# Optimization experiments

Hardware: AMD Instinct MI355X
Metric: run time of the kernel (lower is better)

The kernel has to match this reference:

```python
import jax, jax.numpy as jnp
import numpy as np

C = 1.0          # ball curvature c (manifold k = -c)
RC = 1.0         # sqrt(c)
PROJ_EPS = 4e-3  # geoopt float32 projection eps
NUM_HEADS = 16
B, S, D = 2, 1024, 1024


def _project(x):
    # clip points back inside the Poincare ball
    maxnorm = (1.0 - PROJ_EPS) / RC
    norm = jnp.maximum(jnp.linalg.norm(x, axis=-1, keepdims=True), 1e-15)
    return jnp.where(norm > maxnorm, x / norm * maxnorm, x)


def _poincare_linear(x, z, r, out_split):
    # Unidirectional Poincare MLR (Shimizu et al., HNN++) followed by exp-map back to the ball.
    # x: [..., din]; z: [din, dout]; r: [dout]
    z_norm = jnp.maximum(jnp.linalg.norm(z, axis=0, keepdims=True), 1e-15)  # [1, dout]
    z_unit = z / z_norm
    drcr = 2.0 * RC * r                                    # [dout]
    rcx = RC * x
    cx2 = jnp.sum(rcx * rcx, axis=-1, keepdims=True)       # [..., 1]
    w = 2.0 * (z_norm / RC) * jnp.arcsinh(
        (2.0 * (rcx @ z_unit) * jnp.cosh(drcr) - (1.0 + cx2) * jnp.sinh(drcr))
        / jnp.maximum(1.0 - cx2, 1e-15))
    y = jnp.sinh(RC * w) / RC
    y = y.reshape(y.shape[:-1] + (out_split, y.shape[-1] // out_split))  # [..., H, dh]
    y = _project(y)
    y = y / (1.0 + jnp.sqrt(1.0 + C * jnp.sum(y * y, axis=-1, keepdims=True)))
    return _project(y)


def _dist_matmul(x, y):
    # Pairwise Poincare distance via matmul. x: [..., n, d], y: [..., d, m].
    # dist = (1/sqrt(c)) * arccosh(1 + 2c||x-y||^2 / ((1-c||x||^2)(1-c||y||^2)))
    xy = jnp.matmul(x, y)
    x2 = jnp.sum(x * x, axis=-1, keepdims=True)           # [..., n, 1]
    y2 = jnp.sum(y * y, axis=-2, keepdims=True)           # [..., 1, m]
    num = jnp.maximum(x2 - 2.0 * xy + y2, 1e-15)          # ||x - y||^2
    den = jnp.maximum((1.0 - C * x2) * (1.0 - C * y2), 1e-15)
    return (1.0 / RC) * jnp.arccosh(1.0 + 2.0 * C * num / den)


def _weighted_midpoint_bmm(xs, weights):
    # Weighted Mobius gyromidpoint. xs: [..., n, d], weights: [..., m, n] -> [..., m, d]
    x2 = jnp.sum(xs * xs, axis=-1, keepdims=True)
    gamma = 2.0 / jnp.maximum(1.0 - C * x2, 1e-15)        # conformal factor lambda_x
    denom = jnp.matmul(jnp.abs(weights), gamma - 1.0)     # [..., m, 1]
    nomin = jnp.matmul(weights, gamma * xs)               # [..., m, d]
    two_mean = nomin / jnp.maximum(denom, 1e-10)
    sq = jnp.sum(two_mean * two_mean, axis=-1, keepdims=True)
    a_mean = two_mean / (1.0 + jnp.sqrt(jnp.maximum(1.0 - C * sq, 1e-15)))
    return _project(a_mean)


def setup_inputs() -> dict:
    key = jax.random.key(0)
    ks = jax.random.split(key, 4)
    # points must lie inside the unit ball: ||x|| ~ 0.02*sqrt(D) ~ 0.64
    hidden_states = 0.02 * jax.random.normal(ks[0], (B, S, D), dtype=jnp.float32)
    attention_mask = jnp.zeros((B, 1, 1, S), dtype=jnp.float32)
    scale = 1.0 / np.sqrt(D).astype(np.float32)
    qz = scale * jax.random.normal(ks[1], (D, D), dtype=jnp.float32)
    kz = scale * jax.random.normal(ks[2], (D, D), dtype=jnp.float32)
    vz = scale * jax.random.normal(ks[3], (D, D), dtype=jnp.float32)
    qr = jnp.zeros((D,), jnp.float32)
    kr = jnp.zeros((D,), jnp.float32)
    vr = jnp.zeros((D,), jnp.float32)
    return {"hidden_states": hidden_states, "attention_mask": attention_mask,
            "qz": qz, "qr": qr, "kz": kz, "kr": kr, "vz": vz, "vr": vr}


def reference(hidden_states, attention_mask, qz, qr, kz, kr, vz, vr):
    # self-attention path (encoder_hidden_states is None), eval mode (dropout p=0)
    q = _poincare_linear(hidden_states, qz, qr, NUM_HEADS).transpose(0, 2, 1, 3)  # [B,H,S,dh]
    k = _poincare_linear(hidden_states, kz, kr, NUM_HEADS).transpose(0, 2, 1, 3)
    v = _poincare_linear(hidden_states, vz, vr, NUM_HEADS).transpose(0, 2, 1, 3)
    scores = -_dist_matmul(q, jnp.swapaxes(k, -1, -2)) + attention_mask          # [B,H,S,S]
    probs = jax.nn.softmax(scores, axis=-1)
    ctx = _weighted_midpoint_bmm(v, probs)                                       # [B,H,S,dh]
    b, h, s, dh = ctx.shape
    return ctx.transpose(0, 2, 1, 3).reshape(b, s, h * dh)
```

## Files before the change

kernel.cpp:

```cpp
#include <hip/hip_runtime.h>
#include <math.h>

#define BB 2
#define SS 1024
#define DD 1024
#define NH 16
#define DH 64
#define MAXN 0.996f

typedef __attribute__((ext_vector_type(8))) short bf16x8;
typedef __attribute__((ext_vector_type(4))) float f32x4;

__device__ __forceinline__ float xor_sum16(float v){
  v += __shfl_xor(v, 1, 64);
  v += __shfl_xor(v, 2, 64);
  v += __shfl_xor(v, 4, 64);
  v += __shfl_xor(v, 8, 64);
  return v;
}

__device__ __forceinline__ unsigned short f2bf(float x){
  unsigned u = __builtin_bit_cast(unsigned, x);
  unsigned r = u + 0x7FFFu + ((u >> 16) & 1u);
  return (unsigned short)(r >> 16);
}
__device__ __forceinline__ float bf2f(unsigned short b){
  unsigned u = ((unsigned)b) << 16;
  return __builtin_bit_cast(float, u);
}

__device__ __forceinline__ void async_copy16(const unsigned short* g, unsigned short* s){
  __builtin_amdgcn_global_load_lds(
      (const __attribute__((address_space(1))) unsigned int*)g,
      (__attribute__((address_space(3))) unsigned int*)s,
      16, 0, 0);
}

__global__ __launch_bounds__(256) void col_stats_kernel(
    const float* __restrict__ zq, const float* __restrict__ zk, const float* __restrict__ zv,
    const float* __restrict__ rq, const float* __restrict__ rk, const float* __restrict__ rv,
    float* __restrict__ acol, float* __restrict__ bcol, float* __restrict__ scol)
{
  const int m = blockIdx.y;
  const float* z = (m == 0) ? zq : ((m == 1) ? zk : zv);
  const float* r = (m == 0) ? rq : ((m == 1) ? rk : rv);
  const int col = blockIdx.x * 64 + (threadIdx.x & 63);
  const int slice = threadIdx.x >> 6;
  float acc = 0.0f;
  for (int i = slice * 256; i < slice * 256 + 256; ++i) {
    float t = z[(size_t)i * DD + col]; acc = fmaf(t, t, acc);
  }
  __shared__ float red[4][64];
  red[slice][threadIdx.x & 63] = acc;
  __syncthreads();
  if (slice == 0) {
    const int c = threadIdx.x & 63;
    float a = red[0][c] + red[1][c] + red[2][c] + red[3][c];
    float n = fmaxf(sqrtf(a), 1e-15f);
    float rr = 2.0f * r[col];
    acol[m * DD + col] = 2.0f * coshf(rr) / n;
    bcol[m * DD + col] = sinhf(rr);
    scol[m * DD + col] = 2.0f * n;
  }
}

__global__ __launch_bounds__(256) void row_cx2_kernel(const float* __restrict__ x,
                                                      float* __restrict__ cx2)
{
  const int wave = threadIdx.x >> 6;
  const int lane = threadIdx.x & 63;
  const int row = blockIdx.x * 4 + wave;
  const float* xr = x + (size_t)row * DD;
  float acc = 0.0f;
  for (int i = lane; i < DD; i += 64) { float t = xr[i]; acc = fmaf(t, t, acc); }
  #pragma unroll
  for (int m = 1; m < 64; m <<= 1) acc += __shfl_xor(acc, m, 64);
  if (lane == 0) cx2[row] = acc;
}

__global__ __launch_bounds__(256) void convert_x_kernel(
    const float* __restrict__ x,
    unsigned short* __restrict__ Xhi, unsigned short* __restrict__ Xlo)
{
  const size_t g0 = ((size_t)blockIdx.x * 256 + threadIdx.x) * 8;
  #pragma unroll
  for (int h = 0; h < 2; ++h) {
    float4 v = *(const float4*)(x + g0 + 4 * h);
    float a[4] = {v.x, v.y, v.z, v.w};
    ushort4 hv, lv;
    unsigned short* hp = (unsigned short*)&hv;
    unsigned short* lp = (unsigned short*)&lv;
    #pragma unroll
    for (int j = 0; j < 4; ++j) {
      unsigned short hi = f2bf(a[j]);
      hp[j] = hi;
      lp[j] = f2bf(a[j] - bf2f(hi));
    }
    *(ushort4*)(Xhi + g0 + 4 * h) = hv;
    *(ushort4*)(Xlo + g0 + 4 * h) = lv;
  }
}

__global__ __launch_bounds__(256) void convert_zt_kernel(
    const float* __restrict__ zq, const float* __restrict__ zk, const float* __restrict__ zv,
    unsigned short* __restrict__ ZThi, unsigned short* __restrict__ ZTlo)
{
  const int kt = blockIdx.x, nt = blockIdx.y, mat = blockIdx.z;
  const float* z = (mat == 0) ? zq : ((mat == 1) ? zk : zv);
  const int tid = threadIdx.x;
  __shared__ unsigned T[64][69];

  #pragma unroll
  for (int i = 0; i < 4; ++i) {
    const int g = tid + 256 * i;
    const int kr = g >> 4, nc = (g & 15) * 4;
    float4 v = *(const float4*)(z + (size_t)(kt * 64 + kr) * DD + nt * 64 + nc);
    float a[4] = {v.x, v.y, v.z, v.w};
    #pragma unroll
    for (int j = 0; j < 4; ++j) {
      unsigned short hi = f2bf(a[j]);
      unsigned short lo = f2bf(a[j] - bf2f(hi));
      T[kr][nc + j] = ((unsigned)lo << 16) | (unsigned)hi;
    }
  }
  __syncthreads();
  #pragma unroll
  for (int i = 0; i < 4; ++i) {
    const int g = tid + 256 * i;
    const int nr = g >> 4, kc = (g & 15) * 4;
    ushort4 hv, lv;
    unsigned short* hp = (unsigned short*)&hv;
    unsigned short* lp = (unsigned short*)&lv;
    #pragma unroll
    for (int j = 0; j < 4; ++j) {
      unsigned u = T[kc + j][nr];
      hp[j] = (unsigned short)(u & 0xFFFFu);
      lp[j] = (unsigned short)(u >> 16);
    }
    const size_t ob = ((size_t)mat * DD + nt * 64 + nr) * DD + kt * 64 + kc;
    *(ushort4*)(ZThi + ob) = hv;
    *(ushort4*)(ZTlo + ob) = lv;
  }
}

__global__ __launch_bounds__(256, 3) void gemm_mfma_kernel(
    const unsigned short* __restrict__ Xhi, const unsigned short* __restrict__ Xlo,
    const unsigned short* __restrict__ ZThi, const unsigned short* __restrict__ ZTlo,
    const float* __restrict__ acol, const float* __restrict__ bcol, const float* __restrict__ scol,
    const float* __restrict__ cx2,
    float* __restrict__ Q, float* __restrict__ K, float* __restrict__ GV,
    float* __restrict__ q2, float* __restrict__ k2, float* __restrict__ gm1)
{
  __shared__ unsigned short S[2][12288];

  const int mat = blockIdx.z;
  float* OutM = (mat == 0) ? Q  : ((mat == 1) ? K  : GV);
  float* Stat = (mat == 0) ? q2 : ((mat == 1) ? k2 : gm1);

  const int n0 = blockIdx.x * 128;
  const int m0 = blockIdx.y * 64;
  const int tid = threadIdx.x;
  const int wave = tid >> 6, lane = tid & 63;
  const int tx = lane & 15, quad = lane >> 4;
  const int wrow = wave & 1;
  const int wcol = wave >> 1;

  const int l4r = lane >> 2, l4c = (lane & 3) * 8;
  auto slice_ptr = [&](int si) -> const unsigned short* {
    if (si < 8) {
      const unsigned short* base = (si < 4) ? Xhi : Xlo;
      const int r16 = (si & 3) * 16;
      return base + (size_t)(m0 + r16 + l4r) * DD + l4c;
    } else {
      const unsigned short* base = (si < 16) ? ZThi : ZTlo;
      const int r16 = ((si - 8) & 7) * 16;
      return base + ((size_t)mat * DD + n0 + r16 + l4r) * DD + l4c;
    }
  };
  const int s0 = 6 * wave;
  const unsigned short* p0 = slice_ptr(s0 + 0);
  const unsigned short* p1 = slice_ptr(s0 + 1);
  const unsigned short* p2 = slice_ptr(s0 + 2);
  const unsigned short* p3 = slice_ptr(s0 + 3);
  const unsigned short* p4 = slice_ptr(s0 + 4);
  const unsigned short* p5 = slice_ptr(s0 + 5);
  const int o0 = 512 * (s0 + 0), o1 = 512 * (s0 + 1), o2 = 512 * (s0 + 2);
  const int o3 = 512 * (s0 + 3), o4 = 512 * (s0 + 4), o5 = 512 * (s0 + 5);

  const f32x4 z4 = {0.f, 0.f, 0.f, 0.f};
  f32x4 d00 = z4, d01 = z4, d02 = z4, d03 = z4;
  f32x4 d10 = z4, d11 = z4, d12 = z4, d13 = z4;

  async_copy16(p0, &S[0][o0]); async_copy16(p1, &S[0][o1]); async_copy16(p2, &S[0][o2]);
  async_copy16(p3, &S[0][o3]); async_copy16(p4, &S[0][o4]); async_copy16(p5, &S[0][o5]);
  p0 += 32; p1 += 32; p2 += 32; p3 += 32; p4 += 32; p5 += 32;

  for (int kt = 0; kt < 32; ++kt) {
    __syncthreads();
    if (kt < 31) {
      unsigned short* Bn = S[(kt + 1) & 1];
      async_copy16(p0, Bn + o0); async_copy16(p1, Bn + o1); async_copy16(p2, Bn + o2);
      async_copy16(p3, Bn + o3); async_copy16(p4, Bn + o4); async_copy16(p5, Bn + o5);
      p0 += 32; p1 += 32; p2 += 32; p3 += 32; p4 += 32; p5 += 32;
    }
    const unsigned short* Bc = S[kt & 1];
    const int ar = 32 * wrow + tx;
    bf16x8 a_h0 = *(const bf16x8*)&Bc[ar * 32 + 8 * quad];
    bf16x8 a_l0 = *(const bf16x8*)&Bc[2048 + ar * 32 + 8 * quad];
    bf16x8 a_h1 = *(const bf16x8*)&Bc[(ar + 16) * 32 + 8 * quad];
    bf16x8 a_l1 = *(const bf16x8*)&Bc[2048 + (ar + 16) * 32 + 8 * quad];

#define DO_NB(NB, C0, C1) { \
      const int brow = 16 * (4 * wcol + NB) + tx; \
      bf16x8 b_h = *(const bf16x8*)&Bc[4096 + brow * 32 + 8 * quad]; \
      bf16x8 b_l = *(const bf16x8*)&Bc[8192 + brow * 32 + 8 * quad]; \
      C0 = __builtin_amdgcn_mfma_f32_16x16x32_bf16(a_h0, b_h, C0, 0, 0, 0); \
      C0 = __builtin_amdgcn_mfma_f32_16x16x32_bf16(a_h0, b_l, C0, 0, 0, 0); \
      C0 = __builtin_amdgcn_mfma_f32_16x16x32_bf16(a_l0, b_h, C0, 0, 0, 0); \
      C1 = __builtin_amdgcn_mfma_f32_16x16x32_bf16(a_h1, b_h, C1, 0, 0, 0); \
      C1 = __builtin_amdgcn_mfma_f32_16x16x32_bf16(a_h1, b_l, C1, 0, 0, 0); \
      C1 = __builtin_amdgcn_mfma_f32_16x16x32_bf16(a_l1, b_h, C1, 0, 0, 0); }
    DO_NB(0, d00, d10)
    DO_NB(1, d01, d11)
    DO_NB(2, d02, d12)
    DO_NB(3, d03, d13)
#undef DO_NB
  }

  const int head = blockIdx.x * 2 + wcol;
  #pragma unroll
  for (int mb = 0; mb < 2; ++mb) {
    const f32x4 e0 = mb ? d10 : d00;
    const f32x4 e1 = mb ? d11 : d01;
    const f32x4 e2 = mb ? d12 : d02;
    const f32x4 e3 = mb ? d13 : d03;
    #pragma unroll
    for (int r = 0; r < 4; ++r) {
      const int row = m0 + 32 * wrow + 16 * mb + 4 * quad + r;
      const float c2 = cx2[row];
      const float inv = 1.0f / fmaxf(1.0f - c2, 1e-15f);
      const float onec = 1.0f + c2;
      float yv[4];
      #pragma unroll
      for (int nb = 0; nb < 4; ++nb) {
        const float accv = (nb == 0) ? e0[r] : (nb == 1) ? e1[r] : (nb == 2) ? e2[r] : e3[r];
        const int col = mat * DD + n0 + 64 * wcol + 16 * nb + tx;
        const float u = fmaf(accv, acol[col], -(onec * bcol[col])) * inv;
        const float a = fabsf(u);
        const float t = a + sqrtf(fmaf(a, a, 1.0f));
        const float p = __builtin_amdgcn_exp2f(scol[col] * __builtin_amdgcn_logf(t));
        float y = 0.5f * (p - __builtin_amdgcn_rcpf(p));
        yv[nb] = copysignf(y, u);
      }
      const int b = row >> 10, s = row & 1023;
      float n2 = 0.f;
      #pragma unroll
      for (int j = 0; j < 4; ++j) n2 = fmaf(yv[j], yv[j], n2);
      n2 = xor_sum16(n2);
      float n = fmaxf(sqrtf(n2), 1e-15f);
      float s1 = (n > MAXN) ? (MAXN / n) : 1.0f;
      n2 = n2 * s1 * s1;
      float f = 1.0f / (1.0f + sqrtf(1.0f + n2));
      float fs = s1 * f;
      n2 = n2 * f * f;
      float nb2 = fmaxf(sqrtf(n2), 1e-15f);
      float s2f = (nb2 > MAXN) ? (MAXN / nb2) : 1.0f;
      fs *= s2f;
      n2 = n2 * s2f * s2f;

      const size_t bh = (size_t)(b * NH + head);
      const size_t outbase = (bh * SS + s) * DH;
      if (mat == 2) {
        const float gamma = 2.0f / fmaxf(1.0f - n2, 1e-15f);
        #pragma unroll
        for (int j = 0; j < 4; ++j)
          OutM[outbase + 16 * j + tx] = yv[j] * fs * gamma;
        if (tx == 0) Stat[bh * SS + s] = gamma - 1.0f;
      } else {
        #pragma unroll
        for (int j = 0; j < 4; ++j)
          OutM[outbase + 16 * j + tx] = yv[j] * fs;
        if (tx == 0) Stat[bh * SS + s] = n2;
      }
    }
  }
}

__global__ __launch_bounds__(256) void convert_kernel(
    const float* __restrict__ QKV,
    unsigned short* __restrict__ Qhi, unsigned short* __restrict__ Qlo,
    unsigned short* __restrict__ Khi, unsigned short* __restrict__ Klo,
    unsigned short* __restrict__ GThi, unsigned short* __restrict__ GTlo)
{
  const int st = blockIdx.x, bh = blockIdx.y, mat = blockIdx.z;
  const int tid = threadIdx.x;
  const size_t nQKV = (size_t)BB * NH * SS * DH;
  const float* src = QKV + (size_t)mat * nQKV + ((size_t)bh * SS + st * 64) * DH;
  __shared__ unsigned T[64][69];

  if (mat < 2) {
    unsigned short* dh_ = ((mat == 0) ? Qhi : Khi) + ((size_t)bh * SS + st * 64) * DH;
    unsigned short* dl_ = ((mat == 0) ? Qlo : Klo) + ((size_t)bh * SS + st * 64) * DH;
    #pragma unroll
    for (int i = 0; i < 4; ++i) {
      const int g = tid + 256 * i;
      const int row = g >> 4, c4 = (g & 15) * 4;
      float4 v = *(const float4*)(src + row * DH + c4);
      float a[4] = {v.x, v.y, v.z, v.w};
      ushort4 hv, lv;
      unsigned short* hp = (unsigned short*)&hv;
      unsigned short* lp = (unsigned short*)&lv;
      #pragma unroll
      for (int j = 0; j < 4; ++j) {
        unsigned short hi = f2bf(a[j]);
        hp[j] = hi;
        lp[j] = f2bf(a[j] - bf2f(hi));
      }
      *(ushort4*)(dh_ + row * DH + c4) = hv;
      *(ushort4*)(dl_ + row * DH + c4) = lv;
    }
  } else {
    #pragma unroll
    for (int i = 0; i < 4; ++i) {
      const int g = tid + 256 * i;
      const int row = g >> 4, c4 = (g & 15) * 4;
      float4 v = *(const float4*)(src + row * DH + c4);
      float a[4] = {v.x, v.y, v.z, v.w};
      #pragma unroll
      for (int j = 0; j < 4; ++j) {
        unsigned short hi = f2bf(a[j]);
        unsigned short lo = f2bf(a[j] - bf2f(hi));
        T[row][c4 + j] = ((unsigned)lo << 16) | (unsigned)hi;
      }
    }
    __syncthreads();
    #pragma unroll
    for (int i = 0; i < 4; ++i) {
      const int g = tid + 256 * i;
      const int kb = g & 15, dhr = g >> 4;
      ushort4 hv, lv;
      unsigned short* hp = (unsigned short*)&hv;
      unsigned short* lp = (unsigned short*)&lv;
      #pragma unroll
      for (int j = 0; j < 4; ++j) {
        unsigned u = T[4 * kb + j][dhr];
        hp[j] = (unsigned short)(u & 0xFFFFu);
        lp[j] = (unsigned short)(u >> 16);
      }
      const size_t ob = ((size_t)bh * DH + dhr) * SS + st * 64 + 4 * kb;
      *(ushort4*)(GThi + ob) = hv;
      *(ushort4*)(GTlo + ob) = lv;
    }
  }
}

__global__ __launch_bounds__(256) void flash_attn_kernel(
    const unsigned short* __restrict__ Qhi, const unsigned short* __restrict__ Qlo,
    const unsigned short* __restrict__ Khi, const unsigned short* __restrict__ Klo,
    const unsigned short* __restrict__ GThi, const unsigned short* __restrict__ GTlo,
    const float* __restrict__ q2a, const float* __restrict__ k2a, const float* __restrict__ gm1a,
    const float* __restrict__ mask, float* __restrict__ out)
{
  constexpr int LDK = 72;
  __shared__ unsigned short Ks_hi[64 * LDK];
  __shared__ unsigned short Ks_lo[64 * LDK];
  __shared__ unsigned short Gs_hi[64 * LDK];
  __shared__ unsigned short Gs_lo[64 * LDK];
  __shared__ unsigned short Ps_hi[64 * LDK];
  __shared__ unsigned short Ps_lo[64 * LDK];
  __shared__ float k2s[64], ik2s[64], gm1s[64], ems[64];

  const int qt = blockIdx.x, h = blockIdx.y, b = blockIdx.z;
  const int bh = b * NH + h;
  const int tid = threadIdx.x;
  const int wave = tid >> 6, lane = tid & 63;
  const int tx = lane & 15, quad = lane >> 4;
  const int r0 = qt * 64;

  bf16x8 qa_h[2], qa_l[2];
  {
    const size_t qoff = ((size_t)bh * SS + r0 + 16 * wave + tx) * DH;
    #pragma unroll
    for (int kc = 0; kc < 2; ++kc) {
      qa_h[kc] = *(const bf16x8*)(Qhi + qoff + 32 * kc + 8 * quad);
      qa_l[kc] = *(const bf16x8*)(Qlo + qoff + 32 * kc + 8 * quad);
    }
  }
  float q2r[4], iq2[4];
  #pragma unroll
  for (int r = 0; r < 4; ++r) {
    q2r[r] = q2a[(size_t)bh * SS + r0 + 16 * wave + 4 * quad + r];
    iq2[r] = 2.0f / fmaxf(1.0f - q2r[r], 1e-15f);
  }

  const f32x4 zero4 = {0.f, 0.f, 0.f, 0.f};
  f32x4 oacc[4] = {zero4, zero4, zero4, zero4};
  float dden[4] = {0.f, 0.f, 0.f, 0.f};

  const int c0 = tid, c1 = tid + 256;
  const int sr0 = c0 >> 3, sc0 = (c0 & 7) * 8;
  const int sr1 = c1 >> 3, sc1 = (c1 & 7) * 8;

  const size_t kbase = (size_t)bh * SS * DH;
  const size_t gbase = (size_t)bh * DH * SS;

  uint4 pk_h0 = *(const uint4*)(Khi + kbase + (size_t)sr0 * DH + sc0);
  uint4 pk_h1 = *(const uint4*)(Khi + kbase + (size_t)sr1 * DH + sc1);
  uint4 pk_l0 = *(const uint4*)(Klo + kbase + (size_t)sr0 * DH + sc0);
  uint4 pk_l1 = *(const uint4*)(Klo + kbase + (size_t)sr1 * DH + sc1);
  uint4 pg_h0 = *(const uint4*)(GThi + gbase + (size_t)sr0 * SS + sc0);
  uint4 pg_h1 = *(const uint4*)(GThi + gbase + (size_t)sr1 * SS + sc1);
  uint4 pg_l0 = *(const uint4*)(GTlo + gbase + (size_t)sr0 * SS + sc0);
  uint4 pg_l1 = *(const uint4*)(GTlo + gbase + (size_t)sr1 * SS + sc1);
  float p_k2 = 0.f, p_gm1 = 0.f, p_ms = 0.f;
  if (tid < 64) {
    p_k2  = k2a[(size_t)bh * SS + tid];
    p_gm1 = gm1a[(size_t)bh * SS + tid];
    p_ms  = mask[(size_t)b * SS + tid];
  }

  for (int kt = 0; kt < 16; ++kt) {
    __syncthreads();
    *(uint4*)&Ks_hi[sr0 * LDK + sc0] = pk_h0;
    *(uint4*)&Ks_hi[sr1 * LDK + sc1] = pk_h1;
    *(uint4*)&Ks_lo[sr0 * LDK + sc0] = pk_l0;
    *(uint4*)&Ks_lo[sr1 * LDK + sc1] = pk_l1;
    *(uint4*)&Gs_hi[sr0 * LDK + sc0] = pg_h0;
    *(uint4*)&Gs_hi[sr1 * LDK + sc1] = pg_h1;
    *(uint4*)&Gs_lo[sr0 * LDK + sc0] = pg_l0;
    *(uint4*)&Gs_lo[sr1 * LDK + sc1] = pg_l1;
    if (tid < 64) {
      k2s[tid]  = p_k2;
      ik2s[tid] = 1.0f / fmaxf(1.0f - p_k2, 1e-15f);
      gm1s[tid] = p_gm1;
      ems[tid]  = __expf(p_ms);
    }
    __syncthreads();
    if (kt < 15) {
      const int t1 = (kt + 1) * 64;
      const size_t kb_ = kbase + (size_t)t1 * DH;
      const size_t gb_ = gbase + t1;
      pk_h0 = *(const uint4*)(Khi + kb_ + (size_t)sr0 * DH + sc0);
      pk_h1 = *(const uint4*)(Khi + kb_ + (size_t)sr1 * DH + sc1);
      pk_l0 = *(const uint4*)(Klo + kb_ + (size_t)sr0 * DH + sc0);
      pk_l1 = *(const uint4*)(Klo + kb_ + (size_t)sr1 * DH + sc1);
      pg_h0 = *(const uint4*)(GThi + gb_ + (size_t)sr0 * SS + sc0);
      pg_h1 = *(const uint4*)(GThi + gb_ + (size_t)sr1 * SS + sc1);
      pg_l0 = *(const uint4*)(GTlo + gb_ + (size_t)sr0 * SS + sc0);
      pg_l1 = *(const uint4*)(GTlo + gb_ + (size_t)sr1 * SS + sc1);
      if (tid < 64) {
        p_k2  = k2a[(size_t)bh * SS + t1 + tid];
        p_gm1 = gm1a[(size_t)bh * SS + t1 + tid];
        p_ms  = mask[(size_t)b * SS + t1 + tid];
      }
    }

    f32x4 sacc[4] = {zero4, zero4, zero4, zero4};
    #pragma unroll
    for (int kc = 0; kc < 2; ++kc) {
      const int ko = 32 * kc + 8 * quad;
      #pragma unroll
      for (int nb = 0; nb < 4; ++nb) {
        bf16x8 kh = *(const bf16x8*)&Ks_hi[(16 * nb + tx) * LDK + ko];
        bf16x8 kl = *(const bf16x8*)&Ks_lo[(16 * nb + tx) * LDK + ko];
        sacc[nb] = __builtin_amdgcn_mfma_f32_16x16x32_bf16(qa_h[kc], kh, sacc[nb], 0, 0, 0);
        sacc[nb] = __builtin_amdgcn_mfma_f32_16x16x32_bf16(qa_h[kc], kl, sacc[nb], 0, 0, 0);
        sacc[nb] = __builtin_amdgcn_mfma_f32_16x16x32_bf16(qa_l[kc], kh, sacc[nb], 0, 0, 0);
      }
    }

    float pb[4][4];
    #pragma unroll
    for (int nb = 0; nb < 4; ++nb) {
      const int key = 16 * nb + tx;
      const float k2v = k2s[key], ikv = ik2s[key], emv = ems[key], gmv = gm1s[key];
      #pragma unroll
      for (int r = 0; r < 4; ++r) {
        float sv = sacc[nb][r];
        float num = fmaxf(fmaf(-2.0f, sv, q2r[r] + k2v), 1e-15f);
        float e = num * iq2[r] * ikv;
        float g = fmaf(e, e, e + e);
        float z = 1.0f + e + __builtin_amdgcn_sqrtf(g);
        float w = emv * __builtin_amdgcn_rcpf(z);
        pb[r][nb] = w;
        dden[r] = fmaf(w, gmv, dden[r]);
      }
    }

    #pragma unroll
    for (int r = 0; r < 4; ++r) {
      const int prow = 16 * wave + 4 * quad + r;
      #pragma unroll
      for (int nb = 0; nb < 4; ++nb) {
        float w = pb[r][nb];
        unsigned short hi = f2bf(w);
        unsigned short lo = f2bf(w - bf2f(hi));
        Ps_hi[prow * LDK + 16 * nb + tx] = hi;
        Ps_lo[prow * LDK + 16 * nb + tx] = lo;
      }
    }
    #pragma unroll
    for (int kc = 0; kc < 2; ++kc) {
      const int ko = 32 * kc + 8 * quad;
      bf16x8 ph = *(const bf16x8*)&Ps_hi[(16 * wave + tx) * LDK + ko];
      bf16x8 pl = *(const bf16x8*)&Ps_lo[(16 * wave + tx) * LDK + ko];
      #pragma unroll
      for (int nb = 0; nb < 4; ++nb) {
        bf16x8 gh = *(const bf16x8*)&Gs_hi[(16 * nb + tx) * LDK + ko];
        bf16x8 gl = *(const bf16x8*)&Gs_lo[(16 * nb + tx) * LDK + ko];
        oacc[nb] = __builtin_amdgcn_mfma_f32_16x16x32_bf16(ph, gh, oacc[nb], 0, 0, 0);
        oacc[nb] = __builtin_amdgcn_mfma_f32_16x16x32_bf16(ph, gl, oacc[nb], 0, 0, 0);
        oacc[nb] = __builtin_amdgcn_mfma_f32_16x16x32_bf16(pl, gh, oacc[nb], 0, 0, 0);
      }
    }
  }

  #pragma unroll
  for (int r = 0; r < 4; ++r) {
    float d = fmaxf(xor_sum16(dden[r]), 1e-10f);
    float invd = 1.0f / d;
    float tm[4]; float sq = 0.f;
    #pragma unroll
    for (int nb = 0; nb < 4; ++nb) { tm[nb] = oacc[nb][r] * invd; sq = fmaf(tm[nb], tm[nb], sq); }
    sq = xor_sum16(sq);
    const float f = 1.0f / (1.0f + sqrtf(fmaxf(1.0f - sq, 1e-15f)));
    const float n2 = sq * f * f;
    const float n = fmaxf(sqrtf(n2), 1e-15f);
    const float s2 = (n > MAXN) ? (MAXN / n) : 1.0f;
    const float fs = f * s2;
    const int qrow = r0 + 16 * wave + 4 * quad + r;
    #pragma unroll
    for (int nb = 0; nb < 4; ++nb)
      out[((size_t)(b * SS + qrow)) * DD + h * DH + 16 * nb + tx] = tm[nb] * fs;
  }
}

extern "C" void kernel_launch(void* const* d_in, const int* in_sizes, int n_in,
                              void* d_out, int out_size, void* d_ws, size_t ws_size,
                              hipStream_t stream) {
  const float* hs   = (const float*)d_in[0];
  const float* mask = (const float*)d_in[1];
  const float* qz   = (const float*)d_in[2];
  const float* qr   = (const float*)d_in[3];
  const float* kz   = (const float*)d_in[4];
  const float* kr   = (const float*)d_in[5];
  const float* vz   = (const float*)d_in[6];
  const float* vr   = (const float*)d_in[7];
  float* out = (float*)d_out;

  float* ws = (float*)d_ws;
  const size_t nQKV = (size_t)BB * NH * SS * DH;
  const size_t nStat = (size_t)BB * NH * SS;
  float* Q   = ws;
  float* K   = Q + nQKV;
  float* GV  = K + nQKV;
  float* q2  = GV + nQKV;
  float* k2  = q2 + nStat;
  float* gm1 = k2 + nStat;
  float* acol = gm1 + nStat;
  float* bcol = acol + 3 * DD;
  float* scol = bcol + 3 * DD;
  float* cx2 = scol + 3 * DD;
  unsigned short* bbuf = (unsigned short*)(cx2 + 2048);
  unsigned short* Qhi  = bbuf;
  unsigned short* Qlo  = Qhi  + nQKV;
  unsigned short* Khi  = Qlo  + nQKV;
  unsigned short* Klo  = Khi  + nQKV;
  unsigned short* GThi = Klo  + nQKV;
  unsigned short* GTlo = GThi + nQKV;

  const size_t nX = (size_t)BB * SS * DD;
  const size_t nZ = (size_t)3 * DD * DD;
  unsigned short* Xhi  = bbuf;
  unsigned short* Xlo  = Xhi + nX;
  unsigned short* ZThi = Xlo + nX;
  unsigned short* ZTlo = ZThi + nZ;

  col_stats_kernel<<<dim3(16, 3), 256, 0, stream>>>(qz, kz, vz, qr, kr, vr, acol, bcol, scol);
  row_cx2_kernel<<<dim3(512), 256, 0, stream>>>(hs, cx2);
  convert_x_kernel<<<dim3(1024), 256, 0, stream>>>(hs, Xhi, Xlo);
  convert_zt_kernel<<<dim3(16, 16, 3), 256, 0, stream>>>(qz, kz, vz, ZThi, ZTlo);
  gemm_mfma_kernel<<<dim3(8, 32, 3), 256, 0, stream>>>(
      Xhi, Xlo, ZThi, ZTlo, acol, bcol, scol, cx2, Q, K, GV, q2, k2, gm1);
  convert_kernel<<<dim3(16, BB * NH, 3), 256, 0, stream>>>(
      Q, Qhi, Qlo, Khi, Klo, GThi, GTlo);
  flash_attn_kernel<<<dim3(16, NH, BB), 256, 0, stream>>>(
      Qhi, Qlo, Khi, Klo, GThi, GTlo, q2, k2, gm1, mask, out);
}
```

Measured before the change: 230.7 us.

## Load K and G fragments straight from global into registers, drop LDS staging

The flash attention kernel no longer stages K and the transposed gamma-weighted V tiles through shared memory. Each lane loads its MFMA operand fragments directly from global memory into registers and prefetches the next tile in place, which removes both block barriers per iteration. A new small kernel packs k2, 1/(1-k2), gm1 and exp(mask) into one float4 per key, so the attention loop reads one vector load instead of computing these into shared memory. The cost is many more live registers (launch bounds now ask for 2 blocks), redundant global loads across the four waves that share the same K/G tile, and one extra kernel launch.

```diff
diff --git a/kernel.cpp b/kernel.cpp
--- a/kernel.cpp
+++ b/kernel.cpp
@@ -354,21 +354,30 @@
   }
 }
 
-__global__ __launch_bounds__(256) void flash_attn_kernel(
+__global__ __launch_bounds__(256) void aux_pack_kernel(
+    const float* __restrict__ k2, const float* __restrict__ gm1,
+    const float* __restrict__ mask, float4* __restrict__ aux)
+{
+  const int i = blockIdx.x * 256 + threadIdx.x;
+  const float k2v = k2[i];
+  float4 a;
+  a.x = k2v;
+  a.y = 1.0f / fmaxf(1.0f - k2v, 1e-15f);
+  a.z = gm1[i];
+  a.w = __expf(mask[(i >> 14) * SS + (i & 1023)]);
+  aux[i] = a;
+}
+
+__global__ __launch_bounds__(256, 2) void flash_attn_kernel(
     const unsigned short* __restrict__ Qhi, const unsigned short* __restrict__ Qlo,
     const unsigned short* __restrict__ Khi, const unsigned short* __restrict__ Klo,
     const unsigned short* __restrict__ GThi, const unsigned short* __restrict__ GTlo,
-    const float* __restrict__ q2a, const float* __restrict__ k2a, const float* __restrict__ gm1a,
-    const float* __restrict__ mask, float* __restrict__ out)
+    const float* __restrict__ q2a, const float4* __restrict__ aux,
+    float* __restrict__ out)
 {
   constexpr int LDK = 72;
-  __shared__ unsigned short Ks_hi[64 * LDK];
-  __shared__ unsigned short Ks_lo[64 * LDK];
-  __shared__ unsigned short Gs_hi[64 * LDK];
-  __shared__ unsigned short Gs_lo[64 * LDK];
   __shared__ unsigned short Ps_hi[64 * LDK];
   __shared__ unsigned short Ps_lo[64 * LDK];
-  __shared__ float k2s[64], ik2s[64], gm1s[64], ems[64];
 
   const int qt = blockIdx.x, h = blockIdx.y, b = blockIdx.z;
   const int bh = b * NH + h;
@@ -377,14 +386,13 @@
   const int tx = lane & 15, quad = lane >> 4;
   const int r0 = qt * 64;
 
-  bf16x8 qa_h[2], qa_l[2];
+  bf16x8 qa_h0, qa_l0, qa_h1, qa_l1;
   {
-    const size_t qoff = ((size_t)bh * SS + r0 + 16 * wave + tx) * DH;
-    #pragma unroll
-    for (int kc = 0; kc < 2; ++kc) {
-      qa_h[kc] = *(const bf16x8*)(Qhi + qoff + 32 * kc + 8 * quad);
-      qa_l[kc] = *(const bf16x8*)(Qlo + qoff + 32 * kc + 8 * quad);
-    }
+    const size_t qoff = ((size_t)bh * SS + r0 + 16 * wave + tx) * DH + 8 * quad;
+    qa_h0 = *(const bf16x8*)(Qhi + qoff);
+    qa_l0 = *(const bf16x8*)(Qlo + qoff);
+    qa_h1 = *(const bf16x8*)(Qhi + qoff + 32);
+    qa_l1 = *(const bf16x8*)(Qlo + qoff + 32);
   }
   float q2r[4], iq2[4];
   #pragma unroll
@@ -393,127 +401,142 @@
     iq2[r] = 2.0f / fmaxf(1.0f - q2r[r], 1e-15f);
   }
 
+  const unsigned short* Kh_ = Khi + (size_t)bh * SS * DH + (size_t)tx * DH + 8 * quad;
+  const unsigned short* Kl_ = Klo + (size_t)bh * SS * DH + (size_t)tx * DH + 8 * quad;
+  const unsigned short* Gh_ = GThi + (size_t)bh * DH * SS + (size_t)tx * SS + 8 * quad;
+  const unsigned short* Gl_ = GTlo + (size_t)bh * DH * SS + (size_t)tx * SS + 8 * quad;
+  const float4* auxp = aux + (size_t)bh * SS + tx;
+
   const f32x4 zero4 = {0.f, 0.f, 0.f, 0.f};
   f32x4 oacc[4] = {zero4, zero4, zero4, zero4};
   float dden[4] = {0.f, 0.f, 0.f, 0.f};
 
-  const int c0 = tid, c1 = tid + 256;
-  const int sr0 = c0 >> 3, sc0 = (c0 & 7) * 8;
-  const int sr1 = c1 >> 3, sc1 = (c1 & 7) * 8;
-
-  const size_t kbase = (size_t)bh * SS * DH;
-  const size_t gbase = (size_t)bh * DH * SS;
-
-  uint4 pk_h0 = *(const uint4*)(Khi + kbase + (size_t)sr0 * DH + sc0);
-  uint4 pk_h1 = *(const uint4*)(Khi + kbase + (size_t)sr1 * DH + sc1);
-  uint4 pk_l0 = *(const uint4*)(Klo + kbase + (size_t)sr0 * DH + sc0);
-  uint4 pk_l1 = *(const uint4*)(Klo + kbase + (size_t)sr1 * DH + sc1);
-  uint4 pg_h0 = *(const uint4*)(GThi + gbase + (size_t)sr0 * SS + sc0);
-  uint4 pg_h1 = *(const uint4*)(GThi + gbase + (size_t)sr1 * SS + sc1);
-  uint4 pg_l0 = *(const uint4*)(GTlo + gbase + (size_t)sr0 * SS + sc0);
-  uint4 pg_l1 = *(const uint4*)(GTlo + gbase + (size_t)sr1 * SS + sc1);
-  float p_k2 = 0.f, p_gm1 = 0.f, p_ms = 0.f;
-  if (tid < 64) {
-    p_k2  = k2a[(size_t)bh * SS + tid];
-    p_gm1 = gm1a[(size_t)bh * SS + tid];
-    p_ms  = mask[(size_t)b * SS + tid];
-  }
-
+  uint4 kh0, kh1, kh2, kh3, kh4, kh5, kh6, kh7;
+  uint4 kl0, kl1, kl2, kl3, kl4, kl5, kl6, kl7;
+  uint4 gh0, gh1, gh2, gh3, gh4, gh5, gh6, gh7;
+  uint4 gl0, gl1, gl2, gl3, gl4, gl5, gl6, gl7;
+  float4 ax0, ax1, ax2, ax3;
+
+#define LOADK(T0) { \
+  kh0 = *(const uint4*)(Kh_ + (size_t)((T0) +  0) * DH);      kl0 = *(const uint4*)(Kl_ + (size_t)((T0) +  0) * DH); \
+  kh1 = *(const uint4*)(Kh_ + (size_t)((T0) + 16) * DH);      kl1 = *(const uint4*)(Kl_ + (size_t)((T0) + 16) * DH); \
+  kh2 = *(const uint4*)(Kh_ + (size_t)((T0) + 32) * DH);      kl2 = *(const uint4*)(Kl_ + (size_t)((T0) + 32) * DH); \
+  kh3 = *(const uint4*)(Kh_ + (size_t)((T0) + 48) * DH);      kl3 = *(const uint4*)(Kl_ + (size_t)((T0) + 48) * DH); \
+  kh4 = *(const uint4*)(Kh_ + (size_t)((T0) +  0) * DH + 32); kl4 = *(const uint4*)(Kl_ + (size_t)((T0) +  0) * DH + 32); \
+  kh5 = *(const uint4*)(Kh_ + (size_t)((T0) + 16) * DH + 32); kl5 = *(const uint4*)(Kl_ + (size_t)((T0) + 16) * DH + 32); \
+  kh6 = *(const uint4*)(Kh_ + (size_t)((T0) + 32) * DH + 32); kl6 = *(const uint4*)(Kl_ + (size_t)((T0) + 32) * DH + 32); \
+  kh7 = *(const uint4*)(Kh_ + (size_t)((T0) + 48) * DH + 32); kl7 = *(const uint4*)(Kl_ + (size_t)((T0) + 48) * DH + 32); }
+
+#define LOADG(T0) { \
+  gh0 = *(const uint4*)(Gh_ +  0 * SS + (T0));      gl0 = *(const uint4*)(Gl_ +  0 * SS + (T0)); \
+  gh1 = *(const uint4*)(Gh_ + 16 * SS + (T0));      gl1 = *(const uint4*)(Gl_ + 16 * SS + (T0)); \
+  gh2 = *(const uint4*)(Gh_ + 32 * SS + (T0));      gl2 = *(const uint4*)(Gl_ + 32 * SS + (T0)); \
+  gh3 = *(const uint4*)(Gh_ + 48 * SS + (T0));      gl3 = *(const uint4*)(Gl_ + 48 * SS + (T0)); \
+  gh4 = *(const uint4*)(Gh_ +  0 * SS + (T0) + 32); gl4 = *(const uint4*)(Gl_ +  0 * SS + (T0) + 32); \
+  gh5 = *(const uint4*)(Gh_ + 16 * SS + (T0) + 32); gl5 = *(const uint4*)(Gl_ + 16 * SS + (T0) + 32); \
+  gh6 = *(const uint4*)(Gh_ + 32 * SS + (T0) + 32); gl6 = *(const uint4*)(Gl_ + 32 * SS + (T0) + 32); \
+  gh7 = *(const uint4*)(Gh_ + 48 * SS + (T0) + 32); gl7 = *(const uint4*)(Gl_ + 48 * SS + (T0) + 32); }
+
+#define LOADAUX(T0) { \
+  ax0 = auxp[(T0) +  0]; ax1 = auxp[(T0) + 16]; \
+  ax2 = auxp[(T0) + 32]; ax3 = auxp[(T0) + 48]; }
+
+#define BC(v) (*(const bf16x8*)&(v))
+
+  LOADK(0)
+  LOADG(0)
+  LOADAUX(0)
+
+  #pragma unroll 1
   for (int kt = 0; kt < 16; ++kt) {
-    __syncthreads();
-    *(uint4*)&Ks_hi[sr0 * LDK + sc0] = pk_h0;
-    *(uint4*)&Ks_hi[sr1 * LDK + sc1] = pk_h1;
-    *(uint4*)&Ks_lo[sr0 * LDK + sc0] = pk_l0;
-    *(uint4*)&Ks_lo[sr1 * LDK + sc1] = pk_l1;
-    *(uint4*)&Gs_hi[sr0 * LDK + sc0] = pg_h0;
-    *(uint4*)&Gs_hi[sr1 * LDK + sc1] = pg_h1;
-    *(uint4*)&Gs_lo[sr0 * LDK + sc0] = pg_l0;
-    *(uint4*)&Gs_lo[sr1 * LDK + sc1] = pg_l1;
-    if (tid < 64) {
-      k2s[tid]  = p_k2;
-      ik2s[tid] = 1.0f / fmaxf(1.0f - p_k2, 1e-15f);
-      gm1s[tid] = p_gm1;
-      ems[tid]  = __expf(p_ms);
-    }
-    __syncthreads();
-    if (kt < 15) {
-      const int t1 = (kt + 1) * 64;
-      const size_t kb_ = kbase + (size_t)t1 * DH;
-      const size_t gb_ = gbase + t1;
-      pk_h0 = *(const uint4*)(Khi + kb_ + (size_t)sr0 * DH + sc0);
-      pk_h1 = *(const uint4*)(Khi + kb_ + (size_t)sr1 * DH + sc1);
-      pk_l0 = *(const uint4*)(Klo + kb_ + (size_t)sr0 * DH + sc0);
-      pk_l1 = *(const uint4*)(Klo + kb_ + (size_t)sr1 * DH + sc1);
-      pg_h0 = *(const uint4*)(GThi + gb_ + (size_t)sr0 * SS + sc0);
-      pg_h1 = *(const uint4*)(GThi + gb_ + (size_t)sr1 * SS + sc1);
-      pg_l0 = *(const uint4*)(GTlo + gb_ + (size_t)sr0 * SS + sc0);
-      pg_l1 = *(const uint4*)(GTlo + gb_ + (size_t)sr1 * SS + sc1);
-      if (tid < 64) {
-        p_k2  = k2a[(size_t)bh * SS + t1 + tid];
-        p_gm1 = gm1a[(size_t)bh * SS + t1 + tid];
-        p_ms  = mask[(size_t)b * SS + t1 + tid];
-      }
-    }
-
-    f32x4 sacc[4] = {zero4, zero4, zero4, zero4};
-    #pragma unroll
-    for (int kc = 0; kc < 2; ++kc) {
-      const int ko = 32 * kc + 8 * quad;
-      #pragma unroll
-      for (int nb = 0; nb < 4; ++nb) {
-        bf16x8 kh = *(const bf16x8*)&Ks_hi[(16 * nb + tx) * LDK + ko];
-        bf16x8 kl = *(const bf16x8*)&Ks_lo[(16 * nb + tx) * LDK + ko];
-        sacc[nb] = __builtin_amdgcn_mfma_f32_16x16x32_bf16(qa_h[kc], kh, sacc[nb], 0, 0, 0);
-        sacc[nb] = __builtin_amdgcn_mfma_f32_16x16x32_bf16(qa_h[kc], kl, sacc[nb], 0, 0, 0);
-        sacc[nb] = __builtin_amdgcn_mfma_f32_16x16x32_bf16(qa_l[kc], kh, sacc[nb], 0, 0, 0);
-      }
-    }
-
-    float pb[4][4];
-    #pragma unroll
-    for (int nb = 0; nb < 4; ++nb) {
-      const int key = 16 * nb + tx;
-      const float k2v = k2s[key], ikv = ik2s[key], emv = ems[key], gmv = gm1s[key];
-      #pragma unroll
-      for (int r = 0; r < 4; ++r) {
-        float sv = sacc[nb][r];
-        float num = fmaxf(fmaf(-2.0f, sv, q2r[r] + k2v), 1e-15f);
-        float e = num * iq2[r] * ikv;
-        float g = fmaf(e, e, e + e);
-        float z = 1.0f + e + __builtin_amdgcn_sqrtf(g);
-        float w = emv * __builtin_amdgcn_rcpf(z);
-        pb[r][nb] = w;
-        dden[r] = fmaf(w, gmv, dden[r]);
-      }
-    }
-
-    #pragma unroll
-    for (int r = 0; r < 4; ++r) {
-      const int prow = 16 * wave + 4 * quad + r;
-      #pragma unroll
-      for (int nb = 0; nb < 4; ++nb) {
-        float w = pb[r][nb];
-        unsigned short hi = f2bf(w);
-        unsigned short lo = f2bf(w - bf2f(hi));
-        Ps_hi[prow * LDK + 16 * nb + tx] = hi;
-        Ps_lo[prow * LDK + 16 * nb + tx] = lo;
-      }
-    }
-    #pragma unroll
-    for (int kc = 0; kc < 2; ++kc) {
-      const int ko = 32 * kc + 8 * quad;
-      bf16x8 ph = *(const bf16x8*)&Ps_hi[(16 * wave + tx) * LDK + ko];
-      bf16x8 pl = *(const bf16x8*)&Ps_lo[(16 * wave + tx) * LDK + ko];
-      #pragma unroll
-      for (int nb = 0; nb < 4; ++nb) {
-        bf16x8 gh = *(const bf16x8*)&Gs_hi[(16 * nb + tx) * LDK + ko];
-        bf16x8 gl = *(const bf16x8*)&Gs_lo[(16 * nb + tx) * LDK + ko];
-        oacc[nb] = __builtin_amdgcn_mfma_f32_16x16x32_bf16(ph, gh, oacc[nb], 0, 0, 0);
-        oacc[nb] = __builtin_amdgcn_mfma_f32_16x16x32_bf16(ph, gl, oacc[nb], 0, 0, 0);
-        oacc[nb] = __builtin_amdgcn_mfma_f32_16x16x32_bf16(pl, gh, oacc[nb], 0, 0, 0);
-      }
-    }
-  }
+    f32x4 s0 = zero4, s1 = zero4, s2 = zero4, s3 = zero4;
+    s0 = __builtin_amdgcn_mfma_f32_16x16x32_bf16(qa_h0, BC(kh0), s0, 0, 0, 0);
+    s0 = __builtin_amdgcn_mfma_f32_16x16x32_bf16(qa_h0, BC(kl0), s0, 0, 0, 0);
+    s0 = __builtin_amdgcn_mfma_f32_16x16x32_bf16(qa_l0, BC(kh0), s0, 0, 0, 0);
+    s0 = __builtin_amdgcn_mfma_f32_16x16x32_bf16(qa_h1, BC(kh4), s0, 0, 0, 0);
+    s0 = __builtin_amdgcn_mfma_f32_16x16x32_bf16(qa_h1, BC(kl4), s0, 0, 0, 0);
+    s0 = __builtin_amdgcn_mfma_f32_16x16x32_bf16(qa_l1, BC(kh4), s0, 0, 0, 0);
+    s1 = __builtin_amdgcn_mfma_f32_16x16x32_bf16(qa_h0, BC(kh1), s1, 0, 0, 0);
+    s1 = __builtin_amdgcn_mfma_f32_16x16x32_bf16(qa_h0, BC(kl1), s1, 0, 0, 0);
+    s1 = __builtin_amdgcn_mfma_f32_16x16x32_bf16(qa_l0, BC(kh1), s1, 0, 0, 0);
+    s1 = __builtin_amdgcn_mfma_f32_16x16x32_bf16(qa_h1, BC(kh5), s1, 0, 0, 0);
+    s1 = __builtin_amdgcn_mfma_f32_16x16x32_bf16(qa_h1, BC(kl5), s1, 0, 0, 0);
+    s1 = __builtin_amdgcn_mfma_f32_16x16x32_bf16(qa_l1, BC(kh5), s1, 0, 0, 0);
+    s2 = __builtin_amdgcn_mfma_f32_16x16x32_bf16(qa_h0, BC(kh2), s2, 0, 0, 0);
+    s2 = __builtin_amdgcn_mfma_f32_16x16x32_bf16(qa_h0, BC(kl2), s2, 0, 0, 0);
+    s2 = __builtin_amdgcn_mfma_f32_16x16x32_bf16(qa_l0, BC(kh2), s2, 0, 0, 0);
+    s2 = __builtin_amdgcn_mfma_f32_16x16x32_bf16(qa_h1, BC(kh6), s2, 0, 0, 0);
+    s2 = __builtin_amdgcn_mfma_f32_16x16x32_bf16(qa_h1, BC(kl6), s2, 0, 0, 0);
+    s2 = __builtin_amdgcn_mfma_f32_16x16x32_bf16(qa_l1, BC(kh6), s2, 0, 0, 0);
+    s3 = __builtin_amdgcn_mfma_f32_16x16x32_bf16(qa_h0, BC(kh3), s3, 0, 0, 0);
+    s3 = __builtin_amdgcn_mfma_f32_16x16x32_bf16(qa_h0, BC(kl3), s3, 0, 0, 0);
+    s3 = __builtin_amdgcn_mfma_f32_16x16x32_bf16(qa_l0, BC(kh3), s3, 0, 0, 0);
+    s3 = __builtin_amdgcn_mfma_f32_16x16x32_bf16(qa_h1, BC(kh7), s3, 0, 0, 0);
+    s3 = __builtin_amdgcn_mfma_f32_16x16x32_bf16(qa_h1, BC(kl7), s3, 0, 0, 0);
+    s3 = __builtin_amdgcn_mfma_f32_16x16x32_bf16(qa_l1, BC(kh7), s3, 0, 0, 0);
+
+    const int t1 = (kt + 1) * 64;
+    if (kt < 15) { LOADK(t1) }
+
+#define DIST(NB, SA, AX) { \
+      const float k2v = AX.x, ikv = AX.y, gmv = AX.z, emv = AX.w; \
+      _Pragma("unroll") \
+      for (int r = 0; r < 4; ++r) { \
+        float sv = SA[r]; \
+        float num = fmaxf(fmaf(-2.0f, sv, q2r[r] + k2v), 1e-15f); \
+        float e = num * iq2[r] * ikv; \
+        float g = fmaf(e, e, e + e); \
+        float z = 1.0f + e + __builtin_amdgcn_sqrtf(g); \
+        float w = emv * __builtin_amdgcn_rcpf(z); \
+        dden[r] = fmaf(w, gmv, dden[r]); \
+        unsigned short hi = f2bf(w); \
+        unsigned short lo = f2bf(w - bf2f(hi)); \
+        const int prow = 16 * wave + 4 * quad + r; \
+        Ps_hi[prow * LDK + 16 * NB + tx] = hi; \
+        Ps_lo[prow * LDK + 16 * NB + tx] = lo; \
+      } }
+    DIST(0, s0, ax0)
+    DIST(1, s1, ax1)
+    DIST(2, s2, ax2)
+    DIST(3, s3, ax3)
+#undef DIST
+    if (kt < 15) { LOADAUX(t1) }
+
+    bf16x8 ph0 = *(const bf16x8*)&Ps_hi[(16 * wave + tx) * LDK + 8 * quad];
+    bf16x8 pl0 = *(const bf16x8*)&Ps_lo[(16 * wave + tx) * LDK + 8 * quad];
+    bf16x8 ph1 = *(const bf16x8*)&Ps_hi[(16 * wave + tx) * LDK + 32 + 8 * quad];
+    bf16x8 pl1 = *(const bf16x8*)&Ps_lo[(16 * wave + tx) * LDK + 32 + 8 * quad];
+    oacc[0] = __builtin_amdgcn_mfma_f32_16x16x32_bf16(ph0, BC(gh0), oacc[0], 0, 0, 0);
+    oacc[0] = __builtin_amdgcn_mfma_f32_16x16x32_bf16(ph0, BC(gl0), oacc[0], 0, 0, 0);
+    oacc[0] = __builtin_amdgcn_mfma_f32_16x16x32_bf16(pl0, BC(gh0), oacc[0], 0, 0, 0);
+    oacc[0] = __builtin_amdgcn_mfma_f32_16x16x32_bf16(ph1, BC(gh4), oacc[0], 0, 0, 0);
+    oacc[0] = __builtin_amdgcn_mfma_f32_16x16x32_bf16(ph1, BC(gl4), oacc[0], 0, 0, 0);
+    oacc[0] = __builtin_amdgcn_mfma_f32_16x16x32_bf16(pl1, BC(gh4), oacc[0], 0, 0, 0);
+    oacc[1] = __builtin_amdgcn_mfma_f32_16x16x32_bf16(ph0, BC(gh1), oacc[1], 0, 0, 0);
+    oacc[1] = __builtin_amdgcn_mfma_f32_16x16x32_bf16(ph0, BC(gl1), oacc[1], 0, 0, 0);
+    oacc[1] = __builtin_amdgcn_mfma_f32_16x16x32_bf16(pl0, BC(gh1), oacc[1], 0, 0, 0);
+    oacc[1] = __builtin_amdgcn_mfma_f32_16x16x32_bf16(ph1, BC(gh5), oacc[1], 0, 0, 0);
+    oacc[1] = __builtin_amdgcn_mfma_f32_16x16x32_bf16(ph1, BC(gl5), oacc[1], 0, 0, 0);
+    oacc[1] = __builtin_amdgcn_mfma_f32_16x16x32_bf16(pl1, BC(gh5), oacc[1], 0, 0, 0);
+    oacc[2] = __builtin_amdgcn_mfma_f32_16x16x32_bf16(ph0, BC(gh2), oacc[2], 0, 0, 0);
+    oacc[2] = __builtin_amdgcn_mfma_f32_16x16x32_bf16(ph0, BC(gl2), oacc[2], 0, 0, 0);
+    oacc[2] = __builtin_amdgcn_mfma_f32_16x16x32_bf16(pl0, BC(gh2), oacc[2], 0, 0, 0);
+    oacc[2] = __builtin_amdgcn_mfma_f32_16x16x32_bf16(ph1, BC(gh6), oacc[2], 0, 0, 0);
+    oacc[2] = __builtin_amdgcn_mfma_f32_16x16x32_bf16(ph1, BC(gl6), oacc[2], 0, 0, 0);
+    oacc[2] = __builtin_amdgcn_mfma_f32_16x16x32_bf16(pl1, BC(gh6), oacc[2], 0, 0, 0);
+    oacc[3] = __builtin_amdgcn_mfma_f32_16x16x32_bf16(ph0, BC(gh3), oacc[3], 0, 0, 0);
+    oacc[3] = __builtin_amdgcn_mfma_f32_16x16x32_bf16(ph0, BC(gl3), oacc[3], 0, 0, 0);
+    oacc[3] = __builtin_amdgcn_mfma_f32_16x16x32_bf16(pl0, BC(gh3), oacc[3], 0, 0, 0);
+    oacc[3] = __builtin_amdgcn_mfma_f32_16x16x32_bf16(ph1, BC(gh7), oacc[3], 0, 0, 0);
+    oacc[3] = __builtin_amdgcn_mfma_f32_16x16x32_bf16(ph1, BC(gl7), oacc[3], 0, 0, 0);
+    oacc[3] = __builtin_amdgcn_mfma_f32_16x16x32_bf16(pl1, BC(gh7), oacc[3], 0, 0, 0);
+
+    if (kt < 15) { LOADG(t1) }
+  }
+#undef LOADK
+#undef LOADG
+#undef LOADAUX
+#undef BC
 
   #pragma unroll
   for (int r = 0; r < 4; ++r) {
@@ -561,7 +584,8 @@
   float* bcol = acol + 3 * DD;
   float* scol = bcol + 3 * DD;
   float* cx2 = scol + 3 * DD;
-  unsigned short* bbuf = (unsigned short*)(cx2 + 2048);
+  float4* aux = (float4*)(cx2 + 2048);
+  unsigned short* bbuf = (unsigned short*)(aux + nStat);
   unsigned short* Qhi  = bbuf;
   unsigned short* Qlo  = Qhi  + nQKV;
   unsigned short* Khi  = Qlo  + nQKV;
@@ -584,6 +608,7 @@
       Xhi, Xlo, ZThi, ZTlo, acol, bcol, scol, cx2, Q, K, GV, q2, k2, gm1);
   convert_kernel<<<dim3(16, BB * NH, 3), 256, 0, stream>>>(
       Q, Qhi, Qlo, Khi, Klo, GThi, GTlo);
+  aux_pack_kernel<<<dim3(128), 256, 0, stream>>>(k2, gm1, mask, aux);
   flash_attn_kernel<<<dim3(16, NH, BB), 256, 0, stream>>>(
-      Qhi, Qlo, Khi, Klo, GThi, GTlo, q2, k2, gm1, mask, out);
-}
+      Qhi, Qlo, Khi, Klo, GThi, GTlo, q2, aux, out);
+}
```

Result: slower. 298.8 us (+29.5%).
